# Kernel tuning notes

Measured on AMD Instinct MI355X. Metric: run time of the kernel, lower is better.

## Reference

```python
import jax, jax.numpy as jnp
import numpy as np

EPS = 1e-5

def setup_inputs() -> dict:
    key = jax.random.key(0)
    ks = jax.random.split(key, 8)
    N, C, ST, LT = 32, 2048, 16, 400
    ALPHA, K, BETA, CK = 4, 3, 4, 3
    Cb = C // BETA
    inp = {
        'st_feat': jax.random.normal(ks[0], (N, C, ST, 1, 1), dtype=jnp.float32),
        'lt_feat': jax.random.normal(ks[1], (N, C, LT, 1, 1), dtype=jnp.float32),
        # global branch G: Linear(ST->ST*alpha) -> BN1d -> ReLU -> Linear(->K) -> softmax
        'g_w1': jax.random.normal(ks[2], (ST * ALPHA, ST), dtype=jnp.float32) * 0.02,
        'g_bn_gamma': jnp.ones((ST * ALPHA,), jnp.float32),
        'g_bn_beta': jnp.zeros((ST * ALPHA,), jnp.float32),
        'g_bn_mean': jnp.zeros((ST * ALPHA,), jnp.float32),
        'g_bn_var': jnp.ones((ST * ALPHA,), jnp.float32),
        'g_w2': jax.random.normal(ks[3], (K, ST * ALPHA), dtype=jnp.float32) * 0.02,
        # local branch L: Conv1d(C->C/beta,k=3) -> BN1d -> ReLU -> Conv1d(C/beta->C,1) -> sigmoid
        'l_w1': jax.random.normal(ks[4], (Cb, C, CK), dtype=jnp.float32) * 0.02,
        'l_bn_gamma': jnp.ones((Cb,), jnp.float32),
        'l_bn_beta': jnp.zeros((Cb,), jnp.float32),
        'l_bn_mean': jnp.zeros((Cb,), jnp.float32),
        'l_bn_var': jnp.ones((Cb,), jnp.float32),
        'l_w2': jax.random.normal(ks[5], (C, Cb), dtype=jnp.float32) * 0.02,
    }
    return inp


def reference(st_feat, lt_feat, g_w1, g_bn_gamma, g_bn_beta, g_bn_mean, g_bn_var,
              g_w2, l_w1, l_bn_gamma, l_bn_beta, l_bn_mean, l_bn_var, l_w2):
    N, C, ST = st_feat.shape[:3]
    LT = lt_feat.shape[2]
    K = g_w2.shape[0]
    PAD = 1  # adaptive_convolution_padding; stride = 1
    # ---- global branch: per-(n,c) adaptive kernel (h=w=1 so avgpool is identity)
    st = st_feat.reshape(N * C, ST)                               # [NC, ST]
    h = st @ g_w1.T                                               # [NC, ST*alpha]
    h = (h - g_bn_mean) * jax.lax.rsqrt(g_bn_var + EPS) * g_bn_gamma + g_bn_beta
    h = jax.nn.relu(h)
    conv_kernel = jax.nn.softmax(h @ g_w2.T, axis=-1)             # [NC, K]
    # ---- local branch: channel-temporal sigmoid gate
    lt = lt_feat.reshape(N, C, LT)                                # [N, C, LT]
    x = jax.lax.conv_general_dilated(lt, l_w1, window_strides=(1,),
                                     padding=[(1, 1)],
                                     dimension_numbers=('NCH', 'OIH', 'NCH'))  # [N, C/beta, LT]
    x = (x - l_bn_mean[None, :, None]) * jax.lax.rsqrt(l_bn_var + EPS)[None, :, None] \
        * l_bn_gamma[None, :, None] + l_bn_beta[None, :, None]
    x = jax.nn.relu(x)
    gate = jax.nn.sigmoid(jnp.einsum('oc,nct->not', l_w2, x))     # [N, C, LT]
    new_lt = lt * gate
    # ---- temporal adaptive aggregation: per-(n,c) depthwise 1D conv, K taps
    kern = conv_kernel.reshape(N, C, K)
    xp = jnp.pad(new_lt, ((0, 0), (0, 0), (PAD, PAD)))            # [N, C, LT+2*PAD]
    out_len = LT + 2 * PAD - K + 1                                # == LT for K=3, PAD=1
    out = jnp.zeros((N, C, out_len), dtype=new_lt.dtype)
    for i in range(K):  # K is tiny (3)
        out = out + kern[:, :, i:i + 1] * xp[:, :, i:i + out_len]
    return out.reshape(N, C, out_len, 1, 1)
```

## Files before the change

### kernel.cpp

```cpp
#include <hip/hip_runtime.h>
#include <hip/hip_bf16.h>

#define N_   32
#define C_   2048
#define ST_  16
#define H_   64
#define K_   3
#define CB_  512
#define LT_  400
#define LTP_ 402
#define BK   32
#define TV1  254
#define FNT  12800
#define JW   126
#define NLD  132

using bf16x8 = __attribute__((ext_vector_type(8))) __bf16;
using f32x4  = __attribute__((ext_vector_type(4))) float;
typedef unsigned short ushort_t;

__device__ __forceinline__ unsigned short f2bf(float f) {
    unsigned int u = __float_as_uint(f);
    u = (u + 0x7fffu + ((u >> 16) & 1u)) >> 16;
    return (unsigned short)u;
}
__device__ __forceinline__ float bf2f(unsigned short h) {
    return __uint_as_float(((unsigned int)h) << 16);
}
__device__ __forceinline__ void gload16(const ushort_t* g, ushort_t* l) {
    __builtin_amdgcn_global_load_lds(
        (const __attribute__((address_space(1))) unsigned int*)g,
        (__attribute__((address_space(3))) unsigned int*)l, 16, 0, 0);
}

__global__ __launch_bounds__(256) void k_global(
    const float* __restrict__ st, const float* __restrict__ g_w1,
    const float* __restrict__ gam, const float* __restrict__ bet,
    const float* __restrict__ mean, const float* __restrict__ var,
    const float* __restrict__ g_w2, float* __restrict__ kern) {
    __shared__ float w1[H_][ST_];
    __shared__ float sc[H_], bi[H_];
    __shared__ float w2[K_][H_];
    int tid = threadIdx.x;
    for (int i = tid; i < H_ * ST_; i += 256) w1[i / ST_][i % ST_] = g_w1[i];
    if (tid < H_) {
        float s = gam[tid] * rsqrtf(var[tid] + 1e-5f);
        sc[tid] = s;
        bi[tid] = bet[tid] - mean[tid] * s;
    }
    for (int i = tid; i < K_ * H_; i += 256) w2[i / H_][i % H_] = g_w2[i];
    __syncthreads();
    int row = blockIdx.x * 256 + tid;
    const float* p = st + (size_t)row * ST_;
    float s[ST_];
#pragma unroll
    for (int i = 0; i < ST_; ++i) s[i] = p[i];
    float lg0 = 0.f, lg1 = 0.f, lg2 = 0.f;
    for (int j = 0; j < H_; ++j) {
        float h = 0.f;
#pragma unroll
        for (int i = 0; i < ST_; ++i) h = fmaf(w1[j][i], s[i], h);
        h = fmaxf(fmaf(h, sc[j], bi[j]), 0.f);
        lg0 = fmaf(w2[0][j], h, lg0);
        lg1 = fmaf(w2[1][j], h, lg1);
        lg2 = fmaf(w2[2][j], h, lg2);
    }
    float m = fmaxf(lg0, fmaxf(lg1, lg2));
    float e0 = __expf(lg0 - m), e1 = __expf(lg1 - m), e2 = __expf(lg2 - m);
    float inv = 1.f / (e0 + e1 + e2);
    float4 o = make_float4(e0 * inv, e1 * inv, e2 * inv, 0.f);
    *(float4*)(kern + (size_t)row * 4) = o;
}

__global__ __launch_bounds__(256) void k_transpose(
    const float* __restrict__ lt, ushort_t* __restrict__ ltT) {
    __shared__ float tile[32][33];
    int tt0 = blockIdx.x * 32;
    int cc  = blockIdx.y * 32;
    int n   = blockIdx.z;
    const float* src = lt + ((size_t)n * C_ + cc) * LT_;
    int tx = threadIdx.x & 31, ty = threadIdx.x >> 5;
#pragma unroll
    for (int i = 0; i < 4; ++i) {
        int c = ty + i * 8;
        int t = tt0 + tx;
        tile[c][tx] = (t < LT_) ? src[(size_t)c * LT_ + t] : 0.f;
    }
    __syncthreads();
    int cx  = (threadIdx.x & 15) * 2;
    int tyw = threadIdx.x >> 4;
    unsigned int* dst = (unsigned int*)(ltT + (size_t)n * LTP_ * C_ + cc + cx);
#pragma unroll
    for (int i = 0; i < 2; ++i) {
        int tl = tyw + i * 16;
        int t = tt0 + tl;
        if (t < LT_) {
            unsigned int v = (unsigned int)f2bf(tile[cx][tl]) |
                             ((unsigned int)f2bf(tile[cx + 1][tl]) << 16);
            dst[(size_t)(t + 1) * (C_ / 2)] = v;
        }
    }
}

__global__ __launch_bounds__(256) void k_w1(
    const float* __restrict__ l_w1, ushort_t* __restrict__ w1b,
    ushort_t* __restrict__ ltT) {
    int i = blockIdx.x * 256 + threadIdx.x;
    float a = l_w1[(size_t)i * 3 + 0];
    float b = l_w1[(size_t)i * 3 + 1];
    float c = l_w1[(size_t)i * 3 + 2];
    w1b[0 * (size_t)CB_ * C_ + i] = f2bf(a);
    w1b[1 * (size_t)CB_ * C_ + i] = f2bf(b);
    w1b[2 * (size_t)CB_ * C_ + i] = f2bf(c);
    if (i < N_ * C_) {
        int n = i >> 11, cc = i & (C_ - 1);
        size_t base = (size_t)n * LTP_ * C_;
        ltT[base + cc] = 0;
        ltT[base + (size_t)(LTP_ - 1) * C_ + cc] = 0;
    }
}

__global__ __launch_bounds__(256) void k_w2(
    const float* __restrict__ l_w2, ushort_t* __restrict__ w2b) {
    int i = blockIdx.x * 256 + threadIdx.x;
    w2b[i] = f2bf(l_w2[i]);
}

__global__ __launch_bounds__(512, 2) void k_gemm1(
    const ushort_t* __restrict__ ltT, const ushort_t* __restrict__ w1b,
    const float* __restrict__ bn_g, const float* __restrict__ bn_b,
    const float* __restrict__ bn_m, const float* __restrict__ bn_v,
    ushort_t* __restrict__ Xws) {
    __shared__ __align__(16) ushort_t Asm[3 * 256 * BK + 2 * BK];
    __shared__ __align__(16) ushort_t Bsm[3 * 384 * BK];
    const int tid = threadIdx.x;
    const int mseg = blockIdx.x;
    const int n   = mseg >> 1;
    const int tm  = (mseg & 1) * TV1;
    const int cb0 = blockIdx.y * 128;
    const int lane = tid & 63, lrow = lane & 15, quad = lane >> 4;
    const int wv = tid >> 6;
    const int wvM = wv >> 1, wvN = wv & 1;

    const int srow = lane >> 2;
    const int csrc = (((lane & 3) ^ ((lane >> 3) & 3)) << 3);
    const ushort_t* gA[2];
#pragma unroll
    for (int i = 0; i < 2; ++i) {
        int r = (2 * wv + i) * 16 + srow;
        int gr = tm + r; gr = gr < LTP_ - 1 ? gr : LTP_ - 1;
        gA[i] = ltT + ((size_t)n * LTP_ + gr) * C_ + csrc;
    }
    const ushort_t* gB[3];
#pragma unroll
    for (int j = 0; j < 3; ++j) {
        int rB = (3 * wv + j) * 16 + srow;
        gB[j] = w1b + ((size_t)((rB >> 7) * CB_ + cb0 + (rB & 127))) * C_ + csrc;
    }
    const int sB = lrow * BK + ((quad ^ ((lrow >> 1) & 3)) << 3);
    int sA[3];
#pragma unroll
    for (int k = 0; k < 3; ++k)
        sA[k] = (lrow + k) * BK + ((quad ^ (((lrow + k) >> 1) & 3)) << 3);

    f32x4 acc[4][4];
#pragma unroll
    for (int i = 0; i < 4; ++i)
#pragma unroll
        for (int j = 0; j < 4; ++j) acc[i][j] = (f32x4){0.f, 0.f, 0.f, 0.f};

#define STAGE1(buf)                                                         \
    {                                                                       \
        ushort_t* ad = Asm + (buf) * (256 * BK) + (2 * wv) * (16 * BK);     \
        gload16(gA[0], ad);                                                 \
        gload16(gA[1], ad + 16 * BK);                                       \
        gA[0] += BK; gA[1] += BK;                                           \
        ushort_t* bd = Bsm + (buf) * (384 * BK) + (3 * wv) * (16 * BK);     \
        gload16(gB[0], bd);                                                 \
        gload16(gB[1], bd + 16 * BK);                                       \
        gload16(gB[2], bd + 32 * BK);                                       \
        gB[0] += BK; gB[1] += BK; gB[2] += BK;                              \
    }

    STAGE1(0);
    STAGE1(1);
    int cur = 0, pre = 2;
    for (int s = 0; s < C_ / BK; ++s) {
        if (s < C_ / BK - 1) asm volatile("s_waitcnt vmcnt(5)" ::: "memory");
        else                 asm volatile("s_waitcnt vmcnt(0)" ::: "memory");
        __builtin_amdgcn_sched_barrier(0);
        __builtin_amdgcn_s_barrier();
        __builtin_amdgcn_sched_barrier(0);
        if (s < C_ / BK - 2) {
            STAGE1(pre);
            pre = (pre == 2) ? 0 : pre + 1;
        }
        const ushort_t* Ab = Asm + cur * (256 * BK) + wvM * (64 * BK);
        const ushort_t* Bb = Bsm + cur * (384 * BK) + wvN * (64 * BK) + sB;
        bf16x8 bfr[3][4];
#pragma unroll
        for (int k = 0; k < 3; ++k)
#pragma unroll
            for (int nf = 0; nf < 4; ++nf)
                bfr[k][nf] = *(const bf16x8*)(Bb + k * (128 * BK) + nf * (16 * BK));
        __builtin_amdgcn_s_setprio(1);
#pragma unroll
        for (int mf = 0; mf < 4; ++mf) {
            bf16x8 af[3];
#pragma unroll
            for (int k = 0; k < 3; ++k)
                af[k] = *(const bf16x8*)(Ab + sA[k] + mf * (16 * BK));
#pragma unroll
            for (int nf = 0; nf < 4; ++nf)
#pragma unroll
                for (int k = 0; k < 3; ++k)
                    acc[mf][nf] = __builtin_amdgcn_mfma_f32_16x16x32_bf16(af[k], bfr[k][nf], acc[mf][nf], 0, 0, 0);
        }
        __builtin_amdgcn_s_setprio(0);
        cur = (cur == 2) ? 0 : cur + 1;
    }
#undef STAGE1
    float sc[4], bo[4];
#pragma unroll
    for (int nf = 0; nf < 4; ++nf) {
        int cb = cb0 + wvN * 64 + nf * 16 + lrow;
        float s0 = bn_g[cb] * rsqrtf(bn_v[cb] + 1e-5f);
        sc[nf] = s0;
        bo[nf] = bn_b[cb] - bn_m[cb] * s0;
    }
#pragma unroll
    for (int mf = 0; mf < 4; ++mf) {
#pragma unroll
        for (int r = 0; r < 4; ++r) {
            int local = wvM * 64 + mf * 16 + quad * 4 + r;
            int t = tm + local;
            if (local < TV1 && t < LT_) {
#pragma unroll
                for (int nf = 0; nf < 4; ++nf) {
                    int cb = cb0 + wvN * 64 + nf * 16 + lrow;
                    float v = fmaxf(fmaf(acc[mf][nf][r], sc[nf], bo[nf]), 0.f);
                    Xws[((size_t)n * LT_ + t) * CB_ + cb] = f2bf(v);
                }
            }
        }
    }
}

__global__ __launch_bounds__(256, 3) void k_gemm2(
    const ushort_t* __restrict__ Xws, const ushort_t* __restrict__ w2b,
    const float* __restrict__ lt, const float* __restrict__ kern,
    float* __restrict__ out) {
    __shared__ __align__(16) ushort_t smem[2 * 3 * 128 * BK];
    ushort_t* const Asm = smem;
    ushort_t* const Bsm = smem + 3 * 128 * BK;
    ushort_t* const nlb = smem;
    const int tid = threadIdx.x;
    const int cm  = blockIdx.x * 128;
    const int fnBase = (int)blockIdx.y * JW - 1;
    const int lane = tid & 63, lrow = lane & 15, quad = lane >> 4;
    const int wv = tid >> 6, wvM = wv & 1, wvN = wv >> 1;

    const int srow = lane >> 2;
    const int csrc = (((lane & 3) ^ ((lane >> 3) & 3)) << 3);
    const ushort_t* gA[2];
    const ushort_t* gB[2];
#pragma unroll
    for (int i = 0; i < 2; ++i) {
        int r = (2 * wv + i) * 16 + srow;
        gA[i] = w2b + (size_t)(cm + r) * CB_ + csrc;
        int fr = fnBase + r;
        fr = fr < 0 ? 0 : (fr > FNT - 1 ? FNT - 1 : fr);
        gB[i] = Xws + (size_t)fr * CB_ + csrc;
    }
    const int sOff = lrow * BK + ((quad ^ ((lrow >> 1) & 3)) << 3);

    f32x4 acc[4][4];
#pragma unroll
    for (int i = 0; i < 4; ++i)
#pragma unroll
        for (int j = 0; j < 4; ++j) acc[i][j] = (f32x4){0.f, 0.f, 0.f, 0.f};

#define STAGE2(buf)                                                         \
    {                                                                       \
        ushort_t* ad = Asm + (buf) * (128 * BK) + (2 * wv) * (16 * BK);     \
        ushort_t* bd = Bsm + (buf) * (128 * BK) + (2 * wv) * (16 * BK);     \
        gload16(gA[0], ad);                                                 \
        gload16(gA[1], ad + 16 * BK);                                       \
        gload16(gB[0], bd);                                                 \
        gload16(gB[1], bd + 16 * BK);                                       \
        gA[0] += BK; gA[1] += BK; gB[0] += BK; gB[1] += BK;                 \
    }

    STAGE2(0);
    STAGE2(1);
    int cur = 0, pre = 2;
    for (int s = 0; s < CB_ / BK; ++s) {
        if (s < CB_ / BK - 1) asm volatile("s_waitcnt vmcnt(4)" ::: "memory");
        else                  asm volatile("s_waitcnt vmcnt(0)" ::: "memory");
        __builtin_amdgcn_sched_barrier(0);
        __builtin_amdgcn_s_barrier();
        __builtin_amdgcn_sched_barrier(0);
        if (s < CB_ / BK - 2) {
            STAGE2(pre);
            pre = (pre == 2) ? 0 : pre + 1;
        }
        const ushort_t* Ab = Asm + cur * (128 * BK) + wvM * (64 * BK) + sOff;
        const ushort_t* Bb = Bsm + cur * (128 * BK) + wvN * (64 * BK) + sOff;
        bf16x8 af[4], bfm[4];
#pragma unroll
        for (int mf = 0; mf < 4; ++mf)
            af[mf] = *(const bf16x8*)(Ab + mf * (16 * BK));
#pragma unroll
        for (int nf = 0; nf < 4; ++nf)
            bfm[nf] = *(const bf16x8*)(Bb + nf * (16 * BK));
        __builtin_amdgcn_s_setprio(1);
#pragma unroll
        for (int mf = 0; mf < 4; ++mf)
#pragma unroll
            for (int nf = 0; nf < 4; ++nf)
                acc[mf][nf] = __builtin_amdgcn_mfma_f32_16x16x32_bf16(af[mf], bfm[nf], acc[mf][nf], 0, 0, 0);
        __builtin_amdgcn_s_setprio(0);
        cur = (cur == 2) ? 0 : cur + 1;
    }
#undef STAGE2
    __syncthreads();
#pragma unroll
    for (int mf = 0; mf < 4; ++mf) {
        int cl = wvM * 64 + mf * 16 + quad * 4;
#pragma unroll
        for (int nf = 0; nf < 4; ++nf) {
            int j  = wvN * 64 + nf * 16 + lrow;
            int fn = fnBase + j;
            int fnc = fn < 0 ? 0 : (fn > FNT - 1 ? FNT - 1 : fn);
            int nn = fnc / LT_, t = fnc - nn * LT_;
            const float* ltp = lt + ((size_t)nn * C_ + cm + cl) * LT_ + t;
            unsigned int u01, u23;
            {
                float g0 = 1.f / (1.f + __expf(-acc[mf][nf][0]));
                float g1 = 1.f / (1.f + __expf(-acc[mf][nf][1]));
                float g2 = 1.f / (1.f + __expf(-acc[mf][nf][2]));
                float g3 = 1.f / (1.f + __expf(-acc[mf][nf][3]));
                unsigned short b0 = f2bf(ltp[0] * g0);
                unsigned short b1 = f2bf(ltp[(size_t)LT_] * g1);
                unsigned short b2 = f2bf(ltp[(size_t)2 * LT_] * g2);
                unsigned short b3 = f2bf(ltp[(size_t)3 * LT_] * g3);
                u01 = (unsigned)b0 | ((unsigned)b1 << 16);
                u23 = (unsigned)b2 | ((unsigned)b3 << 16);
            }
            *(uint2*)&nlb[j * NLD + cl] = make_uint2(u01, u23);
        }
    }
    __syncthreads();
#pragma unroll
    for (int mf = 0; mf < 4; ++mf) {
        int cl = wvM * 64 + mf * 16 + quad * 4;
#pragma unroll
        for (int nf = 0; nf < 4; ++nf) {
            int j  = wvN * 64 + nf * 16 + lrow;
            int fn = fnBase + j;
            if (j >= 1 && j <= JW && fn < FNT) {
                int nn = fn / LT_, t = fn - nn * LT_;
                uint2 va = *(const uint2*)&nlb[(j - 1) * NLD + cl];
                uint2 vb = *(const uint2*)&nlb[j * NLD + cl];
                uint2 vc = *(const uint2*)&nlb[(j + 1) * NLD + cl];
                float lft[4] = {bf2f((unsigned short)(va.x & 0xffffu)),
                                bf2f((unsigned short)(va.x >> 16)),
                                bf2f((unsigned short)(va.y & 0xffffu)),
                                bf2f((unsigned short)(va.y >> 16))};
                float ctr[4] = {bf2f((unsigned short)(vb.x & 0xffffu)),
                                bf2f((unsigned short)(vb.x >> 16)),
                                bf2f((unsigned short)(vb.y & 0xffffu)),
                                bf2f((unsigned short)(vb.y >> 16))};
                float rgt[4] = {bf2f((unsigned short)(vc.x & 0xffffu)),
                                bf2f((unsigned short)(vc.x >> 16)),
                                bf2f((unsigned short)(vc.y & 0xffffu)),
                                bf2f((unsigned short)(vc.y >> 16))};
#pragma unroll
                for (int r = 0; r < 4; ++r) {
                    int c = cm + cl + r;
                    float4 kv = *(const float4*)(kern + ((size_t)nn * C_ + c) * 4);
                    float o = kv.y * ctr[r];
                    if (t > 0)       o += kv.x * lft[r];
                    if (t < LT_ - 1) o += kv.z * rgt[r];
                    out[((size_t)nn * C_ + c) * LT_ + t] = o;
                }
            }
        }
    }
}

extern "C" void kernel_launch(void* const* d_in, const int* in_sizes, int n_in,
                              void* d_out, int out_size, void* d_ws, size_t ws_size,
                              hipStream_t stream) {
    const float* st   = (const float*)d_in[0];
    const float* lt   = (const float*)d_in[1];
    const float* g_w1 = (const float*)d_in[2];
    const float* g_bg = (const float*)d_in[3];
    const float* g_bb = (const float*)d_in[4];
    const float* g_bm = (const float*)d_in[5];
    const float* g_bv = (const float*)d_in[6];
    const float* g_w2 = (const float*)d_in[7];
    const float* l_w1 = (const float*)d_in[8];
    const float* l_bg = (const float*)d_in[9];
    const float* l_bb = (const float*)d_in[10];
    const float* l_bm = (const float*)d_in[11];
    const float* l_bv = (const float*)d_in[12];
    const float* l_w2 = (const float*)d_in[13];
    float* out = (float*)d_out;

    char* ws = (char*)d_ws;
    float*    kern = (float*)(ws + 0);
    ushort_t* w1b  = (ushort_t*)(ws + 1048576);
    ushort_t* w2b  = (ushort_t*)(ws + 7340032);
    ushort_t* Xws  = (ushort_t*)(ws + 9437184);
    ushort_t* ltT  = (ushort_t*)(ws + 22544384);

    k_global<<<dim3((N_ * C_) / 256), dim3(256), 0, stream>>>(
        st, g_w1, g_bg, g_bb, g_bm, g_bv, g_w2, kern);
    k_w1<<<dim3((CB_ * C_) / 256), dim3(256), 0, stream>>>(l_w1, w1b, ltT);
    k_w2<<<dim3((C_ * CB_) / 256), dim3(256), 0, stream>>>(l_w2, w2b);
    k_transpose<<<dim3(13, C_ / 32, N_), dim3(256), 0, stream>>>(lt, ltT);
    k_gemm1<<<dim3(64, 4), dim3(512), 0, stream>>>(
        ltT, w1b, l_bg, l_bb, l_bm, l_bv, Xws);
    k_gemm2<<<dim3(C_ / 128, (FNT + JW - 1) / JW), dim3(256), 0, stream>>>(
        Xws, w2b, lt, kern, out);
}
```

Baseline: 442.9 us.

## Vectorize transpose, merge weight-cast kernels, double-buffer gemm2 for higher occupancy

```diff
diff --git a/kernel.cpp b/kernel.cpp
--- a/kernel.cpp
+++ b/kernel.cpp
@@ -74,36 +74,42 @@
 
 __global__ __launch_bounds__(256) void k_transpose(
     const float* __restrict__ lt, ushort_t* __restrict__ ltT) {
-    __shared__ float tile[32][33];
-    int tt0 = blockIdx.x * 32;
+    __shared__ float tile[32][65];
+    int tt0 = blockIdx.x * 64;
     int cc  = blockIdx.y * 32;
     int n   = blockIdx.z;
     const float* src = lt + ((size_t)n * C_ + cc) * LT_;
-    int tx = threadIdx.x & 31, ty = threadIdx.x >> 5;
-#pragma unroll
-    for (int i = 0; i < 4; ++i) {
-        int c = ty + i * 8;
-        int t = tt0 + tx;
-        tile[c][tx] = (t < LT_) ? src[(size_t)c * LT_ + t] : 0.f;
+    int c  = threadIdx.x >> 3;
+    int tq = threadIdx.x & 7;
+#pragma unroll
+    for (int i = 0; i < 2; ++i) {
+        int tl = tq * 4 + i * 32;
+        int t = tt0 + tl;
+        float4 v = make_float4(0.f, 0.f, 0.f, 0.f);
+        if (t < LT_) v = *(const float4*)(src + (size_t)c * LT_ + t);
+        *(float4*)&tile[c][tl] = v;
     }
     __syncthreads();
-    int cx  = (threadIdx.x & 15) * 2;
-    int tyw = threadIdx.x >> 4;
-    unsigned int* dst = (unsigned int*)(ltT + (size_t)n * LTP_ * C_ + cc + cx);
+    int cq = (threadIdx.x & 7) * 4;
+    int tw = threadIdx.x >> 3;
+    ushort_t* dstb = ltT + (size_t)n * LTP_ * C_ + cc + cq;
 #pragma unroll
     for (int i = 0; i < 2; ++i) {
-        int tl = tyw + i * 16;
+        int tl = tw + i * 32;
         int t = tt0 + tl;
         if (t < LT_) {
-            unsigned int v = (unsigned int)f2bf(tile[cx][tl]) |
-                             ((unsigned int)f2bf(tile[cx + 1][tl]) << 16);
-            dst[(size_t)(t + 1) * (C_ / 2)] = v;
-        }
-    }
-}
-
-__global__ __launch_bounds__(256) void k_w1(
-    const float* __restrict__ l_w1, ushort_t* __restrict__ w1b,
+            unsigned int u01 = (unsigned)f2bf(tile[cq + 0][tl]) |
+                               ((unsigned)f2bf(tile[cq + 1][tl]) << 16);
+            unsigned int u23 = (unsigned)f2bf(tile[cq + 2][tl]) |
+                               ((unsigned)f2bf(tile[cq + 3][tl]) << 16);
+            *(uint2*)(dstb + (size_t)(t + 1) * C_) = make_uint2(u01, u23);
+        }
+    }
+}
+
+__global__ __launch_bounds__(256) void k_prep(
+    const float* __restrict__ l_w1, const float* __restrict__ l_w2,
+    ushort_t* __restrict__ w1b, ushort_t* __restrict__ w2b,
     ushort_t* __restrict__ ltT) {
     int i = blockIdx.x * 256 + threadIdx.x;
     float a = l_w1[(size_t)i * 3 + 0];
@@ -112,18 +118,13 @@
     w1b[0 * (size_t)CB_ * C_ + i] = f2bf(a);
     w1b[1 * (size_t)CB_ * C_ + i] = f2bf(b);
     w1b[2 * (size_t)CB_ * C_ + i] = f2bf(c);
+    w2b[i] = f2bf(l_w2[i]);
     if (i < N_ * C_) {
         int n = i >> 11, cc = i & (C_ - 1);
         size_t base = (size_t)n * LTP_ * C_;
         ltT[base + cc] = 0;
         ltT[base + (size_t)(LTP_ - 1) * C_ + cc] = 0;
     }
-}
-
-__global__ __launch_bounds__(256) void k_w2(
-    const float* __restrict__ l_w2, ushort_t* __restrict__ w2b) {
-    int i = blockIdx.x * 256 + threadIdx.x;
-    w2b[i] = f2bf(l_w2[i]);
 }
 
 __global__ __launch_bounds__(512, 2) void k_gemm1(
@@ -246,13 +247,11 @@
     }
 }
 
-__global__ __launch_bounds__(256, 3) void k_gemm2(
+__global__ __launch_bounds__(256, 4) void k_gemm2(
     const ushort_t* __restrict__ Xws, const ushort_t* __restrict__ w2b,
     const float* __restrict__ lt, const float* __restrict__ kern,
     float* __restrict__ out) {
-    __shared__ __align__(16) ushort_t smem[2 * 3 * 128 * BK];
-    ushort_t* const Asm = smem;
-    ushort_t* const Bsm = smem + 3 * 128 * BK;
+    __shared__ __align__(16) ushort_t smem[128 * NLD];
     ushort_t* const nlb = smem;
     const int tid = threadIdx.x;
     const int cm  = blockIdx.x * 128;
@@ -282,8 +281,8 @@
 
 #define STAGE2(buf)                                                         \
     {                                                                       \
-        ushort_t* ad = Asm + (buf) * (128 * BK) + (2 * wv) * (16 * BK);     \
-        ushort_t* bd = Bsm + (buf) * (128 * BK) + (2 * wv) * (16 * BK);     \
+        ushort_t* ad = smem + (buf) * (128 * BK) + (2 * wv) * (16 * BK);    \
+        ushort_t* bd = smem + 8192 + (buf) * (128 * BK) + (2 * wv) * (16 * BK); \
         gload16(gA[0], ad);                                                 \
         gload16(gA[1], ad + 16 * BK);                                       \
         gload16(gB[0], bd);                                                 \
@@ -292,20 +291,12 @@
     }
 
     STAGE2(0);
-    STAGE2(1);
-    int cur = 0, pre = 2;
+    int cur = 0;
     for (int s = 0; s < CB_ / BK; ++s) {
-        if (s < CB_ / BK - 1) asm volatile("s_waitcnt vmcnt(4)" ::: "memory");
-        else                  asm volatile("s_waitcnt vmcnt(0)" ::: "memory");
-        __builtin_amdgcn_sched_barrier(0);
-        __builtin_amdgcn_s_barrier();
-        __builtin_amdgcn_sched_barrier(0);
-        if (s < CB_ / BK - 2) {
-            STAGE2(pre);
-            pre = (pre == 2) ? 0 : pre + 1;
-        }
-        const ushort_t* Ab = Asm + cur * (128 * BK) + wvM * (64 * BK) + sOff;
-        const ushort_t* Bb = Bsm + cur * (128 * BK) + wvN * (64 * BK) + sOff;
+        __syncthreads();
+        if (s + 1 < CB_ / BK) STAGE2(cur ^ 1);
+        const ushort_t* Ab = smem + cur * (128 * BK) + wvM * (64 * BK) + sOff;
+        const ushort_t* Bb = smem + 8192 + cur * (128 * BK) + wvN * (64 * BK) + sOff;
         bf16x8 af[4], bfm[4];
 #pragma unroll
         for (int mf = 0; mf < 4; ++mf)
@@ -320,7 +311,7 @@
             for (int nf = 0; nf < 4; ++nf)
                 acc[mf][nf] = __builtin_amdgcn_mfma_f32_16x16x32_bf16(af[mf], bfm[nf], acc[mf][nf], 0, 0, 0);
         __builtin_amdgcn_s_setprio(0);
-        cur = (cur == 2) ? 0 : cur + 1;
+        cur ^= 1;
     }
 #undef STAGE2
     __syncthreads();
@@ -334,19 +325,16 @@
             int fnc = fn < 0 ? 0 : (fn > FNT - 1 ? FNT - 1 : fn);
             int nn = fnc / LT_, t = fnc - nn * LT_;
             const float* ltp = lt + ((size_t)nn * C_ + cm + cl) * LT_ + t;
-            unsigned int u01, u23;
-            {
-                float g0 = 1.f / (1.f + __expf(-acc[mf][nf][0]));
-                float g1 = 1.f / (1.f + __expf(-acc[mf][nf][1]));
-                float g2 = 1.f / (1.f + __expf(-acc[mf][nf][2]));
-                float g3 = 1.f / (1.f + __expf(-acc[mf][nf][3]));
-                unsigned short b0 = f2bf(ltp[0] * g0);
-                unsigned short b1 = f2bf(ltp[(size_t)LT_] * g1);
-                unsigned short b2 = f2bf(ltp[(size_t)2 * LT_] * g2);
-                unsigned short b3 = f2bf(ltp[(size_t)3 * LT_] * g3);
-                u01 = (unsigned)b0 | ((unsigned)b1 << 16);
-                u23 = (unsigned)b2 | ((unsigned)b3 << 16);
-            }
+            float g0 = 1.f / (1.f + __expf(-acc[mf][nf][0]));
+            float g1 = 1.f / (1.f + __expf(-acc[mf][nf][1]));
+            float g2 = 1.f / (1.f + __expf(-acc[mf][nf][2]));
+            float g3 = 1.f / (1.f + __expf(-acc[mf][nf][3]));
+            unsigned short b0 = f2bf(ltp[0] * g0);
+            unsigned short b1 = f2bf(ltp[(size_t)LT_] * g1);
+            unsigned short b2 = f2bf(ltp[(size_t)2 * LT_] * g2);
+            unsigned short b3 = f2bf(ltp[(size_t)3 * LT_] * g3);
+            unsigned int u01 = (unsigned)b0 | ((unsigned)b1 << 16);
+            unsigned int u23 = (unsigned)b2 | ((unsigned)b3 << 16);
             *(uint2*)&nlb[j * NLD + cl] = make_uint2(u01, u23);
         }
     }
@@ -417,9 +405,9 @@
 
     k_global<<<dim3((N_ * C_) / 256), dim3(256), 0, stream>>>(
         st, g_w1, g_bg, g_bb, g_bm, g_bv, g_w2, kern);
-    k_w1<<<dim3((CB_ * C_) / 256), dim3(256), 0, stream>>>(l_w1, w1b, ltT);
-    k_w2<<<dim3((C_ * CB_) / 256), dim3(256), 0, stream>>>(l_w2, w2b);
-    k_transpose<<<dim3(13, C_ / 32, N_), dim3(256), 0, stream>>>(lt, ltT);
+    k_prep<<<dim3((CB_ * C_) / 256), dim3(256), 0, stream>>>(
+        l_w1, l_w2, w1b, w2b, ltT);
+    k_transpose<<<dim3(7, C_ / 32, N_), dim3(256), 0, stream>>>(lt, ltT);
     k_gemm1<<<dim3(64, 4), dim3(512), 0, stream>>>(
         ltT, w1b, l_bg, l_bb, l_bm, l_bv, Xws);
     k_gemm2<<<dim3(C_ / 128, (FNT + JW - 1) / JW), dim3(256), 0, stream>>>(
```

Measured after the change: 421.6 us. 4.8% less time.
